# Optimization experiments

Measured on AMD Instinct MI355X. Metric: run time of the kernel, lower is better.

## Reference

```python
import jax, jax.numpy as jnp
import numpy as np

HEADS = 8
FEATURE = 512
COMPUTE = 256
SEQ = 512
BATCH = 64


def setup_inputs() -> dict:
    key = jax.random.key(0)
    ks = jax.random.split(key, 10)
    d1 = jax.random.normal(ks[0], (BATCH, FEATURE), dtype=jnp.float32)
    d2 = jax.random.normal(ks[1], (SEQ, BATCH, FEATURE), dtype=jnp.float32)
    # linear1: Linear(FEATURE -> COMPUTE) + ReLU
    w1 = jax.random.normal(ks[2], (FEATURE, COMPUTE), dtype=jnp.float32) * (1.0 / np.sqrt(FEATURE))
    b1 = jnp.zeros((COMPUTE,), dtype=jnp.float32)
    # per-head score params, stacked: ws[i] is [2C, C], ps[i] is [C, 1]
    W = jax.random.normal(ks[3], (HEADS, 2 * COMPUTE, COMPUTE), dtype=jnp.float32)
    P = jax.random.normal(ks[4], (HEADS, COMPUTE), dtype=jnp.float32)
    # value projection weight_v: [FEATURE, COMPUTE]
    wv = jax.random.normal(ks[5], (FEATURE, COMPUTE), dtype=jnp.float32)
    # cc: Linear(COMPUTE*HEADS -> 128) + ReLU
    wcc = jax.random.normal(ks[6], (COMPUTE * HEADS, 128), dtype=jnp.float32) * (1.0 / np.sqrt(COMPUTE * HEADS))
    bcc = jnp.zeros((128,), dtype=jnp.float32)
    return {"d1": d1, "d2": d2, "w1": w1, "b1": b1, "W": W, "P": P,
            "wv": wv, "wcc": wcc, "bcc": bcc, "d2_size": SEQ}


def reference(d1, d2, w1, b1, W, P, wv, wcc, bcc, d2_size):
    S, B, F = d2.shape
    # linear1 on flattened d2 rows -> [S*B, C]
    d3 = jax.nn.relu(d2.reshape(-1, F) @ w1 + b1)
    # linear1 on d1, tiled S times along batch axis -> [S*B, C]
    d4 = jax.nn.relu(d1 @ w1 + b1)            # [B, C]
    d4 = jnp.tile(d4, (S, 1))                  # [S*B, C]
    d5 = jnp.concatenate([d3, d4], axis=1).reshape(S, B, -1)  # [S, B, 2C]
    # value path: tanh(d2 @ weight_v) -> [B, S, C]
    tv = jnp.tanh(jnp.einsum('sbf,fc->sbc', d2, wv)).transpose(1, 0, 2)
    # all heads batched: us = tanh(d5 @ W_h) -> [H, S, B, C]
    us = jnp.tanh(jnp.einsum('sbd,hdc->hsbc', d5, W))
    atts = jnp.einsum('hsbc,hc->hbs', us, P)   # [H, B, S]
    scores = jax.nn.softmax(atts, axis=-1)     # softmax over sequence
    vs = jnp.einsum('hbs,bsc->hbc', scores, tv)  # weighted sum over S -> [H, B, C]
    # torch.cat(vs, dim=1): head-major concat -> [B, H*C]
    vs = vs.transpose(1, 0, 2).reshape(B, -1)
    return jax.nn.relu(vs @ wcc + bcc)         # [B, 128]
```

## Files before the change

### kernel.cpp

```cpp
#include <hip/hip_runtime.h>
#include <cstddef>
#include <cstdint>

#define HH 8
#define FF 512
#define CC 256
#define SS 512
#define BB 64
#define SB (SS*BB)

typedef __attribute__((ext_vector_type(4))) float f32x4;
typedef __attribute__((ext_vector_type(8))) short bf16x8;

typedef __attribute__((address_space(1))) unsigned int gu32_t;
typedef __attribute__((address_space(3))) unsigned int lu32_t;

__device__ __forceinline__ void gld16(const void* gp, void* lp) {
    __builtin_amdgcn_global_load_lds((gu32_t*)gp, (lu32_t*)lp, 16, 0, 0);
}

__device__ __forceinline__ float fast_tanh(float x) {
    float e = __expf(2.0f * x);
    return 1.0f - 2.0f / (e + 1.0f);
}
__device__ __forceinline__ float relu_f(float x) { return fmaxf(x, 0.0f); }

__device__ __forceinline__ unsigned short f2bf(float x) {
    unsigned u = __float_as_uint(x);
    unsigned r = u + 0x7FFFu + ((u >> 16) & 1u);
    return (unsigned short)(r >> 16);
}
__device__ __forceinline__ float bf2f(unsigned short h) {
    return __uint_as_float(((unsigned)h) << 16);
}


__global__ __launch_bounds__(256) void p_prep(
    const float* __restrict__ w1, const float* __restrict__ wv,
    const float* __restrict__ W, const float* __restrict__ d1,
    const float* __restrict__ b1,
    unsigned short* __restrict__ w1ts, unsigned short* __restrict__ wvts,
    unsigned short* __restrict__ Wts, float* __restrict__ d4)
{
    __shared__ float T[64][65];
    __shared__ float As[16][68];
    __shared__ float Bs[16][68];
    const int tid = threadIdx.x;
    const int bid = blockIdx.x;
    if (bid < 192) {
        const float* src;
        unsigned short* dst;
        int kt64, nt;
        if (bid < 64) {
            int m = bid >> 5;
            int t = bid & 31;
            kt64 = t >> 2; nt = t & 3;
            src = m ? wv : w1;
            dst = m ? wvts : w1ts;
        } else {
            int t = bid - 64;
            int h = t >> 4; int tt = t & 15;
            kt64 = tt >> 2; nt = tt & 3;
            src = W + (size_t)h * 2 * CC * CC;
            dst = Wts + (size_t)h * 8 * CC * 64;
        }
        const int k0 = kt64 * 64, n0 = nt * 64;
        #pragma unroll
        for (int jj = 0; jj < 4; ++jj) {
            int i = (tid >> 4) + jj * 16;
            int j = (tid & 15) * 4;
            float4 v = *(const float4*)(src + (size_t)(k0 + i) * CC + n0 + j);
            T[i][j] = v.x; T[i][j+1] = v.y; T[i][j+2] = v.z; T[i][j+3] = v.w;
        }
        __syncthreads();
        {
            const int n_local = tid & 63;
            const int kg = (tid >> 6) * 16;
            const int n_abs = n0 + n_local;
            const int sxn = n_abs & 7;
            #pragma unroll
            for (int j = 0; j < 2; ++j) {
                const int kbase = kg + j * 8;
                const int k_abs = k0 + kbase;
                const int kt = k_abs >> 5;
                const int g = (k_abs >> 3) & 3;
                bf16x8 hv8, lv8;
                #pragma unroll
                for (int q = 0; q < 8; ++q) {
                    float x = T[kbase + q][n_local];
                    unsigned short hx = f2bf(x);
                    hv8[q] = (short)hx;
                    lv8[q] = (short)f2bf(x - bf2f(hx));
                }
                size_t rowo = ((size_t)kt * CC + n_abs) * 64;
                *(bf16x8*)(dst + rowo + (size_t)((2*g + 0) ^ sxn) * 8) = hv8;
                *(bf16x8*)(dst + rowo + (size_t)((2*g + 1) ^ sxn) * 8) = lv8;
            }
        }
    } else {
        const int n0 = (bid - 192) * 64;
        const int tx = tid & 15, ty = tid >> 4;
        const int lm = tid >> 2, lk4 = (tid & 3) * 4;
        const int bk = tid >> 4, bn4 = (tid & 15) * 4;
        float acc[4][4] = {};
        for (int k0 = 0; k0 < FF; k0 += 16) {
            float4 a = *(const float4*)(d1 + (size_t)lm * FF + k0 + lk4);
            As[lk4+0][lm] = a.x; As[lk4+1][lm] = a.y;
            As[lk4+2][lm] = a.z; As[lk4+3][lm] = a.w;
            *(float4*)&Bs[bk][bn4] = *(const float4*)(w1 + (size_t)(k0+bk)*CC + n0 + bn4);
            __syncthreads();
            #pragma unroll
            for (int kk = 0; kk < 16; ++kk) {
                float4 a4 = *(const float4*)&As[kk][ty*4];
                float4 b4 = *(const float4*)&Bs[kk][tx*4];
                float av[4] = {a4.x, a4.y, a4.z, a4.w};
                float bv[4] = {b4.x, b4.y, b4.z, b4.w};
                #pragma unroll
                for (int i = 0; i < 4; ++i)
                    #pragma unroll
                    for (int j = 0; j < 4; ++j)
                        acc[i][j] = fmaf(av[i], bv[j], acc[i][j]);
            }
            __syncthreads();
        }
        #pragma unroll
        for (int i = 0; i < 4; ++i) {
            int row = ty*4 + i;
            #pragma unroll
            for (int j = 0; j < 4; ++j)
                d4[(size_t)row*CC + n0 + tx*4 + j] = relu_f(acc[i][j] + b1[n0 + tx*4 + j]);
        }
    }
}

__global__ __launch_bounds__(256, 2) void k1_main(
    const float* __restrict__ d2,
    const unsigned short* __restrict__ w1ts, const unsigned short* __restrict__ wvts,
    const float* __restrict__ b1,
    const float* __restrict__ d4, const float* __restrict__ W,
    unsigned short* __restrict__ d3s, unsigned short* __restrict__ tv,
    float* __restrict__ e4)
{
    __shared__ __align__(16) unsigned short Abuf[128 * 64];
    __shared__ __align__(16) unsigned short Bbuf[256 * 64];

    const int tid = threadIdx.x;
    const int bid = blockIdx.x;

    if (bid >= 512) {
        float (*As)[68] = (float(*)[68])&Abuf[0];
        float (*Bs)[68] = (float(*)[68])&Bbuf[0];
        const int idx = bid - 512;
        const int n0 = (idx & 3) * 64;
        const int h  = idx >> 2;
        const float* Wh = W + ((size_t)h * 2 * CC + CC) * CC;
        const int tx = tid & 15, ty = tid >> 4;
        const int lm = tid >> 2, lk4 = (tid & 3) * 4;
        const int bk = tid >> 4, bn4 = (tid & 15) * 4;
        float acc[4][4] = {};
        for (int k0 = 0; k0 < CC; k0 += 16) {
            float4 a = *(const float4*)(d4 + (size_t)lm * CC + k0 + lk4);
            As[lk4+0][lm] = a.x; As[lk4+1][lm] = a.y;
            As[lk4+2][lm] = a.z; As[lk4+3][lm] = a.w;
            *(float4*)&Bs[bk][bn4] = *(const float4*)(Wh + (size_t)(k0+bk)*CC + n0 + bn4);
            __syncthreads();
            #pragma unroll
            for (int kk = 0; kk < 16; ++kk) {
                float4 a4 = *(const float4*)&As[kk][ty*4];
                float4 b4 = *(const float4*)&Bs[kk][tx*4];
                float av[4] = {a4.x, a4.y, a4.z, a4.w};
                float bv[4] = {b4.x, b4.y, b4.z, b4.w};
                #pragma unroll
                for (int i = 0; i < 4; ++i)
                    #pragma unroll
                    for (int j = 0; j < 4; ++j)
                        acc[i][j] = fmaf(av[i], bv[j], acc[i][j]);
            }
            __syncthreads();
        }
        #pragma unroll
        for (int i = 0; i < 4; ++i) {
            int b = ty*4 + i;
            #pragma unroll
            for (int j = 0; j < 4; ++j)
                e4[((size_t)h*BB + b)*CC + n0 + tx*4 + j] = acc[i][j];
        }
        return;
    }

    const int cxcd = bid & 7;
    const int jd   = bid >> 3;
    const int path = jd & 1;
    const int xb   = (jd >> 1) * 8 + cxcd;
    const int r0   = xb * 128;
    const int lane = tid & 63, w = tid >> 6;
    const int rowgrp = w & 1, colgrp = w >> 1;
    const int cb = lane & 15, quad = lane >> 4;
    const unsigned short* BT = path ? wvts : w1ts;

    f32x4 acc[4][8];
    f32x4 zero = {0.0f, 0.0f, 0.0f, 0.0f};
    #pragma unroll
    for (int rt = 0; rt < 4; ++rt)
        #pragma unroll
        for (int ct = 0; ct < 8; ++ct) acc[rt][ct] = zero;

    const int ar = tid >> 1, ak = (tid & 1) * 16;
    const int arx = ar & 7;
    const int g0 = ak >> 3;
    const int phi = (2 * quad) ^ (cb & 7);

    for (int k0 = 0; k0 < FF; k0 += 32) {
        const int kt = k0 >> 5;
        {
            const unsigned short* Bsrc = BT + (size_t)kt * (CC * 64);
            #pragma unroll
            for (int i = 0; i < 8; ++i) {
                int chunk = i * 4 + w;
                gld16(Bsrc + (size_t)chunk * 512 + lane * 8, &Bbuf[chunk * 512]);
            }
        }
        {
            const float* s = d2 + (size_t)(r0 + ar) * FF + k0 + ak;
            float v[16];
            *(float4*)&v[0]  = *(const float4*)(s);
            *(float4*)&v[4]  = *(const float4*)(s + 4);
            *(float4*)&v[8]  = *(const float4*)(s + 8);
            *(float4*)&v[12] = *(const float4*)(s + 12);
            bf16x8 vh0, vh1, vl0, vl1;
            #pragma unroll
            for (int j = 0; j < 8; ++j) {
                unsigned short h = f2bf(v[j]);
                vh0[j] = (short)h; vl0[j] = (short)f2bf(v[j] - bf2f(h));
                unsigned short h2 = f2bf(v[j+8]);
                vh1[j] = (short)h2; vl1[j] = (short)f2bf(v[j+8] - bf2f(h2));
            }
            unsigned short* Ar = &Abuf[ar * 64];
            *(bf16x8*)&Ar[((2*g0 + 0) ^ arx) * 8] = vh0;
            *(bf16x8*)&Ar[((2*g0 + 1) ^ arx) * 8] = vl0;
            *(bf16x8*)&Ar[((2*g0 + 2) ^ arx) * 8] = vh1;
            *(bf16x8*)&Ar[((2*g0 + 3) ^ arx) * 8] = vl1;
        }
        __syncthreads();
        bf16x8 ahf[4], alf[4];
        #pragma unroll
        for (int rt = 0; rt < 4; ++rt) {
            const unsigned short* Arow = &Abuf[(rowgrp*64 + rt*16 + cb) * 64];
            ahf[rt] = *(const bf16x8*)&Arow[phi * 8];
            alf[rt] = *(const bf16x8*)&Arow[(phi ^ 1) * 8];
        }
        #pragma unroll
        for (int ct = 0; ct < 8; ++ct) {
            const unsigned short* Brow = &Bbuf[(colgrp*128 + ct*16 + cb) * 64];
            bf16x8 bh = *(const bf16x8*)&Brow[phi * 8];
            bf16x8 bl = *(const bf16x8*)&Brow[(phi ^ 1) * 8];
            #pragma unroll
            for (int rt = 0; rt < 4; ++rt) {
                acc[rt][ct] = __builtin_amdgcn_mfma_f32_16x16x32_bf16(ahf[rt], bh, acc[rt][ct], 0, 0, 0);
                acc[rt][ct] = __builtin_amdgcn_mfma_f32_16x16x32_bf16(ahf[rt], bl, acc[rt][ct], 0, 0, 0);
                acc[rt][ct] = __builtin_amdgcn_mfma_f32_16x16x32_bf16(alf[rt], bh, acc[rt][ct], 0, 0, 0);
            }
        }
        __syncthreads();
    }
    if (path == 0) {
        float bias[8];
        #pragma unroll
        for (int ct = 0; ct < 8; ++ct) bias[ct] = b1[colgrp*128 + ct*16 + cb];
        #pragma unroll
        for (int rt = 0; rt < 4; ++rt) {
            #pragma unroll
            for (int r = 0; r < 4; ++r) {
                int gr = r0 + rowgrp*64 + rt*16 + quad*4 + r;
                int sxr = gr & 7;
                #pragma unroll
                for (int ct = 0; ct < 8; ++ct) {
                    int c = colgrp*128 + ct*16 + cb;
                    float val = relu_f(acc[rt][ct][r] + bias[ct]);
                    unsigned short hx = f2bf(val);
                    unsigned short lx = f2bf(val - bf2f(hx));
                    int kt = c >> 5;
                    int g = (c >> 3) & 3;
                    size_t rowo = ((size_t)kt * SB + gr) * 64;
                    d3s[rowo + (size_t)((2*g + 0) ^ sxr) * 8 + (c & 7)] = hx;
                    d3s[rowo + (size_t)((2*g + 1) ^ sxr) * 8 + (c & 7)] = lx;
                }
            }
        }
    } else {
        #pragma unroll
        for (int rt = 0; rt < 4; ++rt) {
            #pragma unroll
            for (int r = 0; r < 4; ++r) {
                int gr = r0 + rowgrp*64 + rt*16 + quad*4 + r;
                int s = gr >> 6, b = gr & 63;
                #pragma unroll
                for (int ct = 0; ct < 8; ++ct) {
                    int c = colgrp*128 + ct*16 + cb;
                    tv[((size_t)b * SS + s) * CC + c] = f2bf(fast_tanh(acc[rt][ct][r]));
                }
            }
        }
    }
}

__global__ __launch_bounds__(256, 2) void k3_atts(
    const unsigned short* __restrict__ d3s, const unsigned short* __restrict__ Wts,
    const float* __restrict__ e4, const float* __restrict__ P,
    float* __restrict__ atts)
{
    __shared__ __align__(16) unsigned short Abuf[128 * 64];
    __shared__ __align__(16) unsigned short Bbuf[256 * 64];
    float (*red)[128] = (float(*)[128])&Abuf[0];

    const int tid = threadIdx.x;
    const int lane = tid & 63, w = tid >> 6;
    const int bid = blockIdx.x;
    const int cxcd = bid & 7;
    const int jj   = bid >> 3;
    const int h    = jj & 7;
    const int xb   = (jj >> 3) * 8 + cxcd;
    const int r0   = xb * 128;
    const int rowgrp = w & 1, colgrp = w >> 1;
    const int cb = lane & 15, quad = lane >> 4;
    const int phi = (2 * quad) ^ (cb & 7);

    const unsigned short* Wh = Wts + (size_t)h * (8 * CC * 64);

    f32x4 acc[4][8];
    f32x4 zero = {0.0f, 0.0f, 0.0f, 0.0f};
    #pragma unroll
    for (int rt = 0; rt < 4; ++rt)
        #pragma unroll
        for (int ct = 0; ct < 8; ++ct) acc[rt][ct] = zero;

    for (int kt = 0; kt < 8; ++kt) {
        {
            const unsigned short* Asrc = d3s + ((size_t)kt * SB + r0) * 64;
            #pragma unroll
            for (int i = 0; i < 4; ++i) {
                int chunk = i * 4 + w;
                gld16(Asrc + (size_t)chunk * 512 + lane * 8, &Abuf[chunk * 512]);
            }
        }
        {
            const unsigned short* Bsrc = Wh + (size_t)kt * (CC * 64);
            #pragma unroll
            for (int i = 0; i < 8; ++i) {
                int chunk = i * 4 + w;
                gld16(Bsrc + (size_t)chunk * 512 + lane * 8, &Bbuf[chunk * 512]);
            }
        }
        __syncthreads();
        bf16x8 ahf[4], alf[4];
        #pragma unroll
        for (int rt = 0; rt < 4; ++rt) {
            const unsigned short* Arow = &Abuf[(rowgrp*64 + rt*16 + cb) * 64];
            ahf[rt] = *(const bf16x8*)&Arow[phi * 8];
            alf[rt] = *(const bf16x8*)&Arow[(phi ^ 1) * 8];
        }
        #pragma unroll
        for (int ct = 0; ct < 8; ++ct) {
            const unsigned short* Brow = &Bbuf[(colgrp*128 + ct*16 + cb) * 64];
            bf16x8 bh = *(const bf16x8*)&Brow[phi * 8];
            bf16x8 bl = *(const bf16x8*)&Brow[(phi ^ 1) * 8];
            #pragma unroll
            for (int rt = 0; rt < 4; ++rt) {
                acc[rt][ct] = __builtin_amdgcn_mfma_f32_16x16x32_bf16(ahf[rt], bh, acc[rt][ct], 0, 0, 0);
                acc[rt][ct] = __builtin_amdgcn_mfma_f32_16x16x32_bf16(ahf[rt], bl, acc[rt][ct], 0, 0, 0);
                acc[rt][ct] = __builtin_amdgcn_mfma_f32_16x16x32_bf16(alf[rt], bh, acc[rt][ct], 0, 0, 0);
            }
        }
        __syncthreads();
    }
    float Pv[8];
    #pragma unroll
    for (int ct = 0; ct < 8; ++ct) Pv[ct] = P[(size_t)h * CC + colgrp*128 + ct*16 + cb];
    #pragma unroll
    for (int rt = 0; rt < 4; ++rt) {
        #pragma unroll
        for (int r = 0; r < 4; ++r) {
            int b = rt*16 + quad*4 + r;
            const float* e4p = e4 + ((size_t)h * BB + b) * CC + colgrp*128 + cb;
            float part = 0.0f;
            #pragma unroll
            for (int ct = 0; ct < 8; ++ct) {
                float u = acc[rt][ct][r] + e4p[ct*16];
                part = fmaf(Pv[ct], fast_tanh(u), part);
            }
            part += __shfl_xor(part, 1); part += __shfl_xor(part, 2);
            part += __shfl_xor(part, 4); part += __shfl_xor(part, 8);
            if (cb == 0) red[colgrp][rowgrp*64 + b] = part;
        }
    }
    __syncthreads();
    if (tid < 128) {
        float v = red[0][tid] + red[1][tid];
        int gr = r0 + tid;
        int s = gr >> 6, b = gr & 63;
        atts[((size_t)h * BB + b) * SS + s] = v;
    }
}

__global__ __launch_bounds__(256) void k456_out(
    const float* __restrict__ atts, const unsigned short* __restrict__ tv,
    const float* __restrict__ wcc, const float* __restrict__ bcc,
    float* __restrict__ out)
{
    __shared__ float sc[HH][SS];
    __shared__ float red[4][2048];
    const int b = blockIdx.x;
    const int tid = threadIdx.x;
    const int lane = tid & 63, w = tid >> 6;

    for (int i = tid; i < HH*SS; i += 256) {
        int h = i >> 9, s = i & 511;
        sc[h][s] = atts[((size_t)h*BB + b)*SS + s];
    }
    __syncthreads();
    #pragma unroll
    for (int t = 0; t < 2; ++t) {
        int hh = w*2 + t;
        float x[8];
        #pragma unroll
        for (int j = 0; j < 8; ++j) x[j] = sc[hh][j*64 + lane];
        float m = x[0];
        #pragma unroll
        for (int j = 1; j < 8; ++j) m = fmaxf(m, x[j]);
        #pragma unroll
        for (int d = 1; d < 64; d <<= 1) m = fmaxf(m, __shfl_xor(m, d));
        float sum = 0.0f;
        #pragma unroll
        for (int j = 0; j < 8; ++j) { x[j] = __expf(x[j] - m); sum += x[j]; }
        #pragma unroll
        for (int d = 1; d < 64; d <<= 1) sum += __shfl_xor(sum, d);
        float inv = 1.0f / sum;
        #pragma unroll
        for (int j = 0; j < 8; ++j) sc[hh][j*64 + lane] = x[j] * inv;
    }
    __syncthreads();
    {
        const int cl = tid & 63, stripe = tid >> 6;
        const int c0 = cl * 4;
        const unsigned short* tvb = tv + ((size_t)b * SS + stripe * 128) * CC + c0;
        float acc[HH][4] = {};
        for (int si = 0; si < 128; ++si) {
            uint2 u = *(const uint2*)(tvb + (size_t)si * CC);
            float x0 = bf2f((unsigned short)(u.x));
            float x1 = bf2f((unsigned short)(u.x >> 16));
            float x2 = bf2f((unsigned short)(u.y));
            float x3 = bf2f((unsigned short)(u.y >> 16));
            int s = stripe * 128 + si;
            #pragma unroll
            for (int h = 0; h < HH; ++h) {
                float wgt = sc[h][s];
                acc[h][0] = fmaf(wgt, x0, acc[h][0]);
                acc[h][1] = fmaf(wgt, x1, acc[h][1]);
                acc[h][2] = fmaf(wgt, x2, acc[h][2]);
                acc[h][3] = fmaf(wgt, x3, acc[h][3]);
            }
        }
        #pragma unroll
        for (int h = 0; h < HH; ++h)
            #pragma unroll
            for (int j = 0; j < 4; ++j)
                red[stripe][h*256 + c0 + j] = acc[h][j];
    }
    __syncthreads();
    for (int i = tid; i < 2048; i += 256)
        red[0][i] = red[0][i] + red[1][i] + red[2][i] + red[3][i];
    __syncthreads();
    {
        const int n = tid & 127, half = tid >> 7;
        float o = 0.0f;
        const int kbase = half * 1024;
        for (int k = 0; k < 1024; ++k)
            o = fmaf(red[0][kbase + k], wcc[(size_t)(kbase + k) * 128 + n], o);
        float* r2 = &sc[0][0];
        r2[half * 128 + n] = o;
    }
    __syncthreads();
    if (tid < 128)
        out[(size_t)b * 128 + tid] = relu_f(sc[0][tid] + sc[0][128 + tid] + bcc[tid]);
}

extern "C" void kernel_launch(void* const* d_in, const int* in_sizes, int n_in,
                              void* d_out, int out_size, void* d_ws, size_t ws_size,
                              hipStream_t stream)
{
    (void)in_sizes; (void)n_in; (void)out_size; (void)ws_size;
    const float* d1  = (const float*)d_in[0];
    const float* d2  = (const float*)d_in[1];
    const float* w1  = (const float*)d_in[2];
    const float* b1  = (const float*)d_in[3];
    const float* W   = (const float*)d_in[4];
    const float* P   = (const float*)d_in[5];
    const float* wv  = (const float*)d_in[6];
    const float* wcc = (const float*)d_in[7];
    const float* bcc = (const float*)d_in[8];
    float* out = (float*)d_out;

    char* p = (char*)d_ws;
    unsigned short* d3s  = (unsigned short*)p; p += (size_t)8 * SB * 64 * 2;
    unsigned short* tv   = (unsigned short*)p; p += (size_t)SB * CC * 2;
    unsigned short* w1ts = (unsigned short*)p; p += (size_t)16 * CC * 64 * 2;
    unsigned short* wvts = (unsigned short*)p; p += (size_t)16 * CC * 64 * 2;
    unsigned short* Wts  = (unsigned short*)p; p += (size_t)HH * 8 * CC * 64 * 2;
    float* d4   = (float*)p;  p += (size_t)BB * CC * 4;
    float* e4   = (float*)p;  p += (size_t)HH * BB * CC * 4;
    float* atts = (float*)p;  p += (size_t)HH * BB * SS * 4;

    p_prep   <<<dim3(196),       256, 0, stream>>>(w1, wv, W, d1, b1,
                  w1ts, wvts, Wts, d4);
    k1_main  <<<dim3(544),       256, 0, stream>>>(d2, w1ts, wvts, b1, d4, W,
                  d3s, tv, e4);
    k3_atts  <<<dim3(2048),      256, 0, stream>>>(d3s, Wts, e4, P, atts);
    k456_out <<<dim3(BB),        256, 0, stream>>>(atts, tv, wcc, bcc, out);
}
```

Before: 351.5 us.

## Stage GEMM epilogue through LDS for coalesced 16-byte stores of d3s and tv

```diff
diff --git a/kernel.cpp b/kernel.cpp
--- a/kernel.cpp
+++ b/kernel.cpp
@@ -141,15 +141,16 @@
     unsigned short* __restrict__ d3s, unsigned short* __restrict__ tv,
     float* __restrict__ e4)
 {
-    __shared__ __align__(16) unsigned short Abuf[128 * 64];
-    __shared__ __align__(16) unsigned short Bbuf[256 * 64];
+    __shared__ __align__(16) unsigned short SH[24576];
+    unsigned short* const Abuf = SH;
+    unsigned short* const Bbuf = SH + 8192;
 
     const int tid = threadIdx.x;
     const int bid = blockIdx.x;
 
     if (bid >= 512) {
-        float (*As)[68] = (float(*)[68])&Abuf[0];
-        float (*Bs)[68] = (float(*)[68])&Bbuf[0];
+        float (*As)[68] = (float(*)[68])&SH[0];
+        float (*Bs)[68] = (float(*)[68])&SH[8192];
         const int idx = bid - 512;
         const int n0 = (idx & 3) * 64;
         const int h  = idx >> 2;
@@ -263,42 +264,72 @@
         }
         __syncthreads();
     }
+
     if (path == 0) {
         float bias[8];
         #pragma unroll
         for (int ct = 0; ct < 8; ++ct) bias[ct] = b1[colgrp*128 + ct*16 + cb];
-        #pragma unroll
-        for (int rt = 0; rt < 4; ++rt) {
-            #pragma unroll
-            for (int r = 0; r < 4; ++r) {
-                int gr = r0 + rowgrp*64 + rt*16 + quad*4 + r;
-                int sxr = gr & 7;
+        unsigned short* Lp = SH + colgrp * 9216;
+        #pragma unroll
+        for (int it = 0; it < 4; ++it) {
+            __syncthreads();
+            #pragma unroll
+            for (int rt = 0; rt < 4; ++rt)
                 #pragma unroll
-                for (int ct = 0; ct < 8; ++ct) {
-                    int c = colgrp*128 + ct*16 + cb;
-                    float val = relu_f(acc[rt][ct][r] + bias[ct]);
-                    unsigned short hx = f2bf(val);
-                    unsigned short lx = f2bf(val - bf2f(hx));
-                    int kt = c >> 5;
-                    int g = (c >> 3) & 3;
-                    size_t rowo = ((size_t)kt * SB + gr) * 64;
-                    d3s[rowo + (size_t)((2*g + 0) ^ sxr) * 8 + (c & 7)] = hx;
-                    d3s[rowo + (size_t)((2*g + 1) ^ sxr) * 8 + (c & 7)] = lx;
+                for (int r = 0; r < 4; ++r) {
+                    int row = rowgrp*64 + rt*16 + quad*4 + r;
+                    int sx = row & 7;
+                    #pragma unroll
+                    for (int t = 0; t < 2; ++t) {
+                        float val = relu_f(acc[rt][2*it + t][r] + bias[2*it + t]);
+                        unsigned short hx = f2bf(val);
+                        unsigned short lx = f2bf(val - bf2f(hx));
+                        int cl = t*16 + cb;
+                        int g = cl >> 3, c7 = cl & 7;
+                        Lp[row*72 + (((2*g + 0) ^ sx) << 3) + c7] = hx;
+                        Lp[row*72 + (((2*g + 1) ^ sx) << 3) + c7] = lx;
+                    }
                 }
+            __syncthreads();
+            #pragma unroll
+            for (int q = 0; q < 8; ++q) {
+                int idx = q*256 + tid;
+                int pp  = idx >> 10;
+                int rc  = idx & 1023;
+                int row = rc >> 3;
+                int ch  = rc & 7;
+                bf16x8 v = *(const bf16x8*)&SH[pp*9216 + row*72 + ch*8];
+                unsigned short* dst = d3s + ((size_t)(pp*4 + it) * SB + r0 + row) * 64;
+                *(bf16x8*)&dst[ch*8] = v;
             }
         }
     } else {
-        #pragma unroll
-        for (int rt = 0; rt < 4; ++rt) {
-            #pragma unroll
-            for (int r = 0; r < 4; ++r) {
-                int gr = r0 + rowgrp*64 + rt*16 + quad*4 + r;
-                int s = gr >> 6, b = gr & 63;
+        unsigned short* Lp = SH + colgrp * 6144;
+        #pragma unroll
+        for (int it = 0; it < 4; ++it) {
+            __syncthreads();
+            #pragma unroll
+            for (int rt = 0; rt < 4; ++rt)
                 #pragma unroll
-                for (int ct = 0; ct < 8; ++ct) {
-                    int c = colgrp*128 + ct*16 + cb;
-                    tv[((size_t)b * SS + s) * CC + c] = f2bf(fast_tanh(acc[rt][ct][r]));
+                for (int r = 0; r < 4; ++r) {
+                    int row = rowgrp*64 + rt*16 + quad*4 + r;
+                    #pragma unroll
+                    for (int t = 0; t < 2; ++t) {
+                        int cl = t*16 + cb;
+                        Lp[row*48 + cl] = f2bf(fast_tanh(acc[rt][2*it + t][r]));
+                    }
                 }
+            __syncthreads();
+            #pragma unroll
+            for (int q = 0; q < 4; ++q) {
+                int idx = q*256 + tid;
+                int pp  = idx >> 9;
+                int rc  = idx & 511;
+                int row = rc >> 2;
+                int ch  = rc & 3;
+                bf16x8 v = *(const bf16x8*)&SH[pp*6144 + row*48 + ch*8];
+                unsigned short* dst = tv + (size_t)(r0 + row) * CC + (pp*4 + it)*32;
+                *(bf16x8*)&dst[ch*8] = v;
             }
         }
     }
@@ -442,10 +473,10 @@
     {
         const int cl = tid & 63, stripe = tid >> 6;
         const int c0 = cl * 4;
-        const unsigned short* tvb = tv + ((size_t)b * SS + stripe * 128) * CC + c0;
+        const unsigned short* tvb = tv + ((size_t)(stripe * 128) * BB + b) * CC + c0;
         float acc[HH][4] = {};
         for (int si = 0; si < 128; ++si) {
-            uint2 u = *(const uint2*)(tvb + (size_t)si * CC);
+            uint2 u = *(const uint2*)(tvb + (size_t)si * BB * CC);
             float x0 = bf2f((unsigned short)(u.x));
             float x1 = bf2f((unsigned short)(u.x >> 16));
             float x2 = bf2f((unsigned short)(u.y));
```

Measured after the change: 357.8 us. No clear change (+1.8%).
